# Optimization experiments

Hardware: AMD Instinct MI355X
Metric: run time of the kernel (lower is better)

## Reference

```python
import jax, jax.numpy as jnp
import numpy as np

NEG_SLOPE = 0.2  # PyG GATConv default leaky_relu slope


def gat_layer(x, src, dst, W, a_src, a_dst, bias, heads, d, concat):
    # x: [N, in_dim]; src/dst: [E] (edges flow src -> dst, self-loops included)
    N = x.shape[0]
    h = (x @ W).reshape(N, heads, d)                      # [N, H, D]
    alpha_src = jnp.einsum('nhd,hd->nh', h, a_src)        # [N, H]
    alpha_dst = jnp.einsum('nhd,hd->nh', h, a_dst)        # [N, H]
    e = jax.nn.leaky_relu(alpha_src[src] + alpha_dst[dst], NEG_SLOPE)  # [E, H]
    # softmax over incoming edges of each destination node (segment softmax)
    m = jax.ops.segment_max(e, dst, num_segments=N)       # [N, H]
    ex = jnp.exp(e - m[dst])
    s = jax.ops.segment_sum(ex, dst, num_segments=N)      # [N, H]
    alpha = ex / s[dst]                                   # [E, H]
    msg = h[src] * alpha[..., None]                       # [E, H, D]
    out = jax.ops.segment_sum(msg, dst, num_segments=N)   # [N, H, D]
    out = out.reshape(N, heads * d) if concat else out.mean(axis=1)
    return out + bias


def setup_inputs() -> dict:
    key = jax.random.key(0)
    ks = jax.random.split(key, 12)
    N, E = 10000, 320000
    in_dim, hidden, heads, out_dim = 256, 64, 4, 40
    x = jax.random.normal(ks[0], (N, in_dim), dtype=jnp.float32)
    edge_index = jax.random.randint(ks[1], (2, E), 0, N, dtype=jnp.int64)
    s = 0.1
    return {
        'x': x,
        'edge_index': edge_index,
        'W1': jax.random.normal(ks[2], (in_dim, heads * hidden), jnp.float32) * s,
        'att_src1': jax.random.normal(ks[3], (heads, hidden), jnp.float32) * s,
        'att_dst1': jax.random.normal(ks[4], (heads, hidden), jnp.float32) * s,
        'bias1': jnp.zeros((heads * hidden,), jnp.float32),
        'W2': jax.random.normal(ks[5], (heads * hidden, out_dim), jnp.float32) * s,
        'att_src2': jax.random.normal(ks[6], (1, out_dim), jnp.float32) * s,
        'att_dst2': jax.random.normal(ks[7], (1, out_dim), jnp.float32) * s,
        'bias2': jnp.zeros((out_dim,), jnp.float32),
    }


def reference(x, edge_index, W1, att_src1, att_dst1, bias1, W2, att_src2, att_dst2, bias2):
    N = x.shape[0]
    # PyG GATConv adds self-loops by default
    loop = jnp.arange(N, dtype=edge_index.dtype)
    src = jnp.concatenate([edge_index[0], loop])
    dst = jnp.concatenate([edge_index[1], loop])
    h = gat_layer(x, src, dst, W1, att_src1, att_dst1, bias1, heads=4, d=64, concat=True)
    h = jax.nn.relu(h)
    out = gat_layer(h, src, dst, W2, att_src2, att_dst2, bias2, heads=1, d=40, concat=False)
    return jax.nn.log_softmax(out, axis=1)
```

## Files before the change

kernel.cpp:

```cpp
#include <hip/hip_runtime.h>
#include <hip/hip_bf16.h>
#include <math.h>

#define IN_DIM 256
#define C1 256
#define H1 4
#define OUT_DIM 40
#define W2PAD 48
#define NEG_SLOPE 0.2f
#define DSTRIDE 128

typedef __attribute__((ext_vector_type(8))) short bf16x8;
typedef __attribute__((ext_vector_type(4))) float f32x4;
typedef __attribute__((ext_vector_type(2))) float f32x2;

#define XS_LD 264

__device__ __forceinline__ unsigned short f2bf(float f) {
    union { float f; unsigned u; } c; c.f = f;
    unsigned r = c.u + 0x7fffu + ((c.u >> 16) & 1u);
    return (unsigned short)(r >> 16);
}

__device__ __forceinline__ unsigned char f2fp8(float f) {
    return (unsigned char)__builtin_amdgcn_cvt_pk_fp8_f32(f, 0.f, 0, false);
}

__device__ __forceinline__ float sel4(float4 v, int h) {
    float r = v.x;
    r = (h == 1) ? v.y : r;
    r = (h == 2) ? v.z : r;
    r = (h == 3) ? v.w : r;
    return r;
}

__device__ __forceinline__ float leaky(float v) {
    return (v >= 0.0f) ? v : NEG_SLOPE * v;
}

__global__ void k_prep(int* __restrict__ fill, const float* __restrict__ W1,
                       unsigned short* __restrict__ W1t, const float* __restrict__ W2,
                       unsigned short* __restrict__ W2t, const float* __restrict__ a_src2,
                       const float* __restrict__ a_dst2, float* __restrict__ w2s,
                       float* __restrict__ w2d, int N) {
    int t = threadIdx.x;
    int g = blockIdx.x * 256 + t;
    if (g < N) fill[g] = 0;
    if (g < C1) {
        float s = 0.0f, d = 0.0f;
#pragma unroll
        for (int j = 0; j < OUT_DIM; ++j) {
            float w = W2[g * OUT_DIM + j];
            s += w * a_src2[j];
            d += w * a_dst2[j];
        }
        w2s[g] = s;
        w2d[g] = d;
    }
    if (g < W2PAD * C1) {
        int j = g >> 8, k = g & 255;
        W2t[g] = (j < OUT_DIM) ? f2bf(W2[k * OUT_DIM + j]) : 0;
    }
    __shared__ float s32[32][33];
    int b = blockIdx.x;
    int r0 = (b >> 3) * 32;
    int c0 = (b & 7) * 32;
    for (int i = t; i < 1024; i += 256) {
        int lr = i >> 5, lc = i & 31;
        s32[lr][lc] = W1[(r0 + lr) * 256 + c0 + lc];
    }
    __syncthreads();
    for (int i = t; i < 1024; i += 256) {
        int oc = i >> 5, ok = i & 31;
        W1t[(c0 + oc) * 256 + r0 + ok] = f2bf(s32[ok][oc]);
    }
}

__global__ void __launch_bounds__(256) k_fused1(
    const float* __restrict__ x, const unsigned short* __restrict__ W1t,
    const float* __restrict__ a_src, const float* __restrict__ a_dst,
    unsigned char* __restrict__ h1, float* __restrict__ as1, float* __restrict__ ad1,
    const int* __restrict__ ei, int* __restrict__ fill, unsigned short* __restrict__ srcs,
    int N, int E, int ET, int G1) {
    __shared__ unsigned short xs[64 * XS_LD];
    int t = threadIdx.x;

    if (blockIdx.x >= G1) {
        int e = (blockIdx.x - G1) * 256 + t;
        if (e < ET) {
            int s, d;
            if (e < E) { s = ei[e]; d = ei[E + e]; }
            else       { s = e - E; d = s; }
            int pos = atomicAdd(&fill[d], 1);
            srcs[(d << 7) + pos] = (unsigned short)s;
        }
        return;
    }

    int n0 = blockIdx.x * 64;
    for (int i = t; i < 4096; i += 256) {
        int r = i >> 6, c4 = i & 63;
        int n = n0 + r;
        float4 v = (n < N) ? ((const float4*)x)[(size_t)n * 64 + c4]
                           : make_float4(0.f, 0.f, 0.f, 0.f);
        uint2 pk;
        pk.x = (unsigned)f2bf(v.x) | ((unsigned)f2bf(v.y) << 16);
        pk.y = (unsigned)f2bf(v.z) | ((unsigned)f2bf(v.w) << 16);
        *((uint2*)&xs[r * XS_LD + c4 * 4]) = pk;
    }
    __syncthreads();

    int wv = t >> 6, lane = t & 63;
    int quad = lane >> 4, ln = lane & 15;

    f32x4 acc[4][4];
#pragma unroll
    for (int mt = 0; mt < 4; ++mt)
#pragma unroll
        for (int nt = 0; nt < 4; ++nt) acc[mt][nt] = (f32x4){0.f, 0.f, 0.f, 0.f};

#pragma unroll
    for (int kb = 0; kb < 8; ++kb) {
        bf16x8 af[4], bf[4];
#pragma unroll
        for (int mt = 0; mt < 4; ++mt)
            af[mt] = *((bf16x8*)&xs[(mt * 16 + ln) * XS_LD + kb * 32 + quad * 8]);
#pragma unroll
        for (int nt = 0; nt < 4; ++nt)
            bf[nt] = *((const bf16x8*)(W1t + ((wv * 64 + nt * 16 + ln) * 256 + kb * 32 + quad * 8)));
#pragma unroll
        for (int mt = 0; mt < 4; ++mt)
#pragma unroll
            for (int nt = 0; nt < 4; ++nt)
                acc[mt][nt] = __builtin_amdgcn_mfma_f32_16x16x32_bf16(af[mt], bf[nt], acc[mt][nt], 0, 0, 0);
    }

    float asv[4], adv[4];
#pragma unroll
    for (int nt = 0; nt < 4; ++nt) {
        int col = wv * 64 + nt * 16 + ln;
        asv[nt] = a_src[col];
        adv[nt] = a_dst[col];
    }
#pragma unroll
    for (int mt = 0; mt < 4; ++mt) {
        float ds[4] = {0.f, 0.f, 0.f, 0.f};
        float dd[4] = {0.f, 0.f, 0.f, 0.f};
#pragma unroll
        for (int nt = 0; nt < 4; ++nt) {
            int col = wv * 64 + nt * 16 + ln;
#pragma unroll
            for (int r = 0; r < 4; ++r) {
                int node = n0 + mt * 16 + quad * 4 + r;
                float v = acc[mt][nt][r];
                if (node < N) h1[(size_t)node * C1 + col] = f2fp8(v);
                ds[r] += v * asv[nt];
                dd[r] += v * adv[nt];
            }
        }
#pragma unroll
        for (int r = 0; r < 4; ++r) {
            float vs = ds[r], vd = dd[r];
#pragma unroll
            for (int o = 1; o < 16; o <<= 1) {
                vs += __shfl_xor(vs, o);
                vd += __shfl_xor(vd, o);
            }
            if (ln == 0) {
                int node = n0 + mt * 16 + quad * 4 + r;
                if (node < N) {
                    as1[node * H1 + wv] = vs;
                    ad1[node * H1 + wv] = vd;
                }
            }
        }
    }
}

__global__ void __launch_bounds__(256) k_node1(
    const int* __restrict__ fill, const unsigned short* __restrict__ srcs,
    const float* __restrict__ as1f, const float* __restrict__ ad1f,
    const unsigned char* __restrict__ h1, const float* __restrict__ bias1,
    const float* __restrict__ w2s, const float* __restrict__ w2d,
    unsigned short* __restrict__ agg1b, float* __restrict__ as2,
    float* __restrict__ ad2, int N) {
    int w = threadIdx.x >> 6, lane = threadIdx.x & 63;
    int n = blockIdx.x * 4 + w;
    if (n >= N) return;
    __shared__ float4 es[4][64];
    int start = n << 7;
    int end = start + fill[n];
    const float4* as4 = (const float4*)as1f;
    float4 adn = ((const float4*)ad1f)[n];
    int h = lane >> 4;
    const float* esw = (const float*)&es[w][0];

    float4 S4 = make_float4(0.f, 0.f, 0.f, 0.f);
    float ac0 = 0.f, ac1 = 0.f, ac2 = 0.f, ac3 = 0.f;

    for (int c = start; c < end; c += 64) {
        int cnt = min(64, end - c);
        int idx = c + lane;
        int sreg = (idx < end) ? (int)srcs[idx] : 0;
        float4 ex = make_float4(0.f, 0.f, 0.f, 0.f);
        if (idx < end) {
            float4 a = as4[sreg];
            ex.x = __expf(leaky(a.x + adn.x));
            ex.y = __expf(leaky(a.y + adn.y));
            ex.z = __expf(leaky(a.z + adn.z));
            ex.w = __expf(leaky(a.w + adn.w));
        }
        S4.x += ex.x; S4.y += ex.y; S4.z += ex.z; S4.w += ex.w;
        es[w][lane] = ex;

        int i = 0;
        for (; i + 7 < cnt; i += 8) {
            int s[8]; float a[8]; unsigned r[8];
#pragma unroll
            for (int k = 0; k < 8; ++k) {
                s[k] = __shfl(sreg, i + k);
                a[k] = esw[(i + k) * 4 + h];
            }
#pragma unroll
            for (int k = 0; k < 8; ++k)
                r[k] = ((const unsigned*)(h1 + (size_t)s[k] * C1))[lane];
#pragma unroll
            for (int k = 0; k < 8; ++k) {
                f32x2 lo = __builtin_amdgcn_cvt_pk_f32_fp8(r[k], false);
                f32x2 hi = __builtin_amdgcn_cvt_pk_f32_fp8(r[k], true);
                ac0 += a[k] * lo.x;
                ac1 += a[k] * lo.y;
                ac2 += a[k] * hi.x;
                ac3 += a[k] * hi.y;
            }
        }
        for (; i < cnt; ++i) {
            int s0 = __shfl(sreg, i);
            float a0 = esw[i * 4 + h];
            unsigned r0 = ((const unsigned*)(h1 + (size_t)s0 * C1))[lane];
            f32x2 lo = __builtin_amdgcn_cvt_pk_f32_fp8(r0, false);
            f32x2 hi = __builtin_amdgcn_cvt_pk_f32_fp8(r0, true);
            ac0 += a0 * lo.x;
            ac1 += a0 * lo.y;
            ac2 += a0 * hi.x;
            ac3 += a0 * hi.y;
        }
    }

#pragma unroll
    for (int o = 32; o > 0; o >>= 1) {
        S4.x += __shfl_xor(S4.x, o);
        S4.y += __shfl_xor(S4.y, o);
        S4.z += __shfl_xor(S4.z, o);
        S4.w += __shfl_xor(S4.w, o);
    }
    float iS = 1.0f / sel4(S4, h);
    float4 b = ((const float4*)bias1)[lane];
    float v0 = fmaxf(ac0 * iS + b.x, 0.f);
    float v1 = fmaxf(ac1 * iS + b.y, 0.f);
    float v2 = fmaxf(ac2 * iS + b.z, 0.f);
    float v3 = fmaxf(ac3 * iS + b.w, 0.f);
    uint2 pk;
    pk.x = (unsigned)f2bf(v0) | ((unsigned)f2bf(v1) << 16);
    pk.y = (unsigned)f2bf(v2) | ((unsigned)f2bf(v3) << 16);
    ((uint2*)(agg1b + (size_t)n * C1))[lane] = pk;

    float4 ws = ((const float4*)w2s)[lane];
    float4 wd = ((const float4*)w2d)[lane];
    float ps = v0 * ws.x + v1 * ws.y + v2 * ws.z + v3 * ws.w;
    float pd = v0 * wd.x + v1 * wd.y + v2 * wd.z + v3 * wd.w;
#pragma unroll
    for (int o = 32; o > 0; o >>= 1) {
        ps += __shfl_xor(ps, o);
        pd += __shfl_xor(pd, o);
    }
    if (lane == 0) { as2[n] = ps; ad2[n] = pd; }
}

__global__ void __launch_bounds__(256) k_gemm2m(
    const unsigned short* __restrict__ agg1b, const unsigned short* __restrict__ W2t,
    unsigned short* __restrict__ h2b, int N) {
    int t = threadIdx.x;
    int wv = t >> 6, lane = t & 63;
    int quad = lane >> 4, ln = lane & 15;
    int n0 = blockIdx.x * 64;
    int mrow = n0 + wv * 16 + ln;

    f32x4 acc[3];
#pragma unroll
    for (int nt = 0; nt < 3; ++nt) acc[nt] = (f32x4){0.f, 0.f, 0.f, 0.f};

#pragma unroll
    for (int kb = 0; kb < 8; ++kb) {
        bf16x8 af = *((const bf16x8*)(agg1b + (size_t)mrow * C1 + kb * 32 + quad * 8));
#pragma unroll
        for (int nt = 0; nt < 3; ++nt) {
            bf16x8 bfr = *((const bf16x8*)(W2t + ((nt * 16 + ln) * C1 + kb * 32 + quad * 8)));
            acc[nt] = __builtin_amdgcn_mfma_f32_16x16x32_bf16(af, bfr, acc[nt], 0, 0, 0);
        }
    }
#pragma unroll
    for (int nt = 0; nt < 3; ++nt) {
        int col = nt * 16 + ln;
        if (col < OUT_DIM) {
#pragma unroll
            for (int r = 0; r < 4; ++r) {
                int node = n0 + wv * 16 + quad * 4 + r;
                if (node < N) h2b[(size_t)node * OUT_DIM + col] = f2bf(acc[nt][r]);
            }
        }
    }
}

__global__ void __launch_bounds__(256) k_node2(
    const int* __restrict__ fill, const unsigned short* __restrict__ srcs,
    const float* __restrict__ as2, const float* __restrict__ ad2,
    const unsigned short* __restrict__ h2b, const float* __restrict__ bias2,
    float* __restrict__ out, int N) {
    int w = threadIdx.x >> 6, lane = threadIdx.x & 63;
    int n = blockIdx.x * 4 + w;
    if (n >= N) return;
    int start = n << 7;
    int end = start + fill[n];
    float adn = ad2[n];
    float S = 0.f, acc0 = 0.f, acc1 = 0.f;
    bool act = lane < 20;

    for (int c = start; c < end; c += 64) {
        int cnt = min(64, end - c);
        int idx = c + lane;
        int sreg = (idx < end) ? (int)srcs[idx] : 0;
        float ex = (idx < end) ? __expf(leaky(as2[sreg] + adn)) : 0.f;
        S += ex;
        int i = 0;
        for (; i + 3 < cnt; i += 4) {
            int su[4]; float al[4]; unsigned rw[4];
#pragma unroll
            for (int k = 0; k < 4; ++k) {
                su[k] = __shfl(sreg, i + k);
                al[k] = __shfl(ex, i + k);
            }
#pragma unroll
            for (int k = 0; k < 4; ++k)
                rw[k] = act ? *(const unsigned*)(h2b + (size_t)su[k] * OUT_DIM + lane * 2) : 0u;
#pragma unroll
            for (int k = 0; k < 4; ++k) {
                acc0 += al[k] * __uint_as_float(rw[k] << 16);
                acc1 += al[k] * __uint_as_float(rw[k] & 0xffff0000u);
            }
        }
        for (; i < cnt; ++i) {
            int su0 = __shfl(sreg, i);
            float al0 = __shfl(ex, i);
            unsigned rw0 = act ? *(const unsigned*)(h2b + (size_t)su0 * OUT_DIM + lane * 2) : 0u;
            acc0 += al0 * __uint_as_float(rw0 << 16);
            acc1 += al0 * __uint_as_float(rw0 & 0xffff0000u);
        }
    }
#pragma unroll
    for (int o = 32; o > 0; o >>= 1) S += __shfl_xor(S, o);

    float v0 = act ? (acc0 / S + bias2[lane * 2]) : -INFINITY;
    float v1 = act ? (acc1 / S + bias2[lane * 2 + 1]) : -INFINITY;
    float mx = fmaxf(v0, v1);
#pragma unroll
    for (int o = 16; o > 0; o >>= 1) mx = fmaxf(mx, __shfl_xor(mx, o));
    float e0 = act ? __expf(v0 - mx) : 0.f;
    float e1 = act ? __expf(v1 - mx) : 0.f;
    float esum = e0 + e1;
#pragma unroll
    for (int o = 16; o > 0; o >>= 1) esum += __shfl_xor(esum, o);
    if (act) {
        float l = mx + logf(esum);
        out[(size_t)n * OUT_DIM + lane * 2]     = v0 - l;
        out[(size_t)n * OUT_DIM + lane * 2 + 1] = v1 - l;
    }
}

extern "C" void kernel_launch(void* const* d_in, const int* in_sizes, int n_in,
                              void* d_out, int out_size, void* d_ws, size_t ws_size,
                              hipStream_t stream) {
    const float* x        = (const float*)d_in[0];
    const int*   ei       = (const int*)d_in[1];
    const float* W1       = (const float*)d_in[2];
    const float* att_src1 = (const float*)d_in[3];
    const float* att_dst1 = (const float*)d_in[4];
    const float* bias1    = (const float*)d_in[5];
    const float* W2       = (const float*)d_in[6];
    const float* att_src2 = (const float*)d_in[7];
    const float* att_dst2 = (const float*)d_in[8];
    const float* bias2    = (const float*)d_in[9];
    float* out = (float*)d_out;

    const int N  = in_sizes[0] / IN_DIM;
    const int E  = in_sizes[1] / 2;
    const int ET = E + N;
    const int Npad = (N + 63) & ~63;

    char* base = (char*)d_ws;
    auto alloc = [&](size_t bytes) {
        char* p = base;
        base += (bytes + 255) & ~(size_t)255;
        return p;
    };
    unsigned char*  h1    = (unsigned char*)alloc((size_t)N * C1);
    unsigned short* W1t   = (unsigned short*)alloc((size_t)C1 * C1 * 2);
    unsigned short* W2t   = (unsigned short*)alloc((size_t)W2PAD * C1 * 2);
    unsigned short* agg1b = (unsigned short*)alloc((size_t)Npad * C1 * 2);
    unsigned short* h2b   = (unsigned short*)alloc((size_t)N * OUT_DIM * 2);
    float* as1   = (float*)alloc((size_t)N * H1 * 4);
    float* ad1   = (float*)alloc((size_t)N * H1 * 4);
    float* as2   = (float*)alloc((size_t)N * 4);
    float* ad2   = (float*)alloc((size_t)N * 4);
    float* w2s   = (float*)alloc((size_t)C1 * 4);
    float* w2d   = (float*)alloc((size_t)C1 * 4);
    int* fill    = (int*)alloc((size_t)N * 4);
    unsigned short* srcs = (unsigned short*)alloc((size_t)N * DSTRIDE * 2);

    const int G1 = (N + 63) / 64;
    const int GS = (ET + 255) / 256;

    k_prep<<<64, 256, 0, stream>>>(fill, W1, W1t, W2, W2t, att_src2, att_dst2, w2s, w2d, N);
    k_fused1<<<G1 + GS, 256, 0, stream>>>(x, W1t, att_src1, att_dst1, h1, as1, ad1,
                                          ei, fill, srcs, N, E, ET, G1);
    k_node1<<<(N + 3) / 4, 256, 0, stream>>>(fill, srcs, as1, ad1, h1, bias1, w2s, w2d,
                                             agg1b, as2, ad2, N);
    k_gemm2m<<<(N + 63) / 64, 256, 0, stream>>>(agg1b, W2t, h2b, N);
    k_node2<<<(N + 3) / 4, 256, 0, stream>>>(fill, srcs, as2, ad2, h2b, bias2, out, N);
}
```

Baseline: 149.6 us.

## Pad fill counters, batch edge scatter per thread, stage h1 stores through LDS

Spreads the per-node atomic fill counters to one every 64 bytes to cut atomic contention and false sharing between neighbouring nodes. Each scatter thread now handles four edges, so fewer scatter blocks are launched. The fp8 h1 tile is written to shared memory first and then stored to global memory as coalesced 16-byte vectors instead of scattered byte stores. The cost is a 16x larger fill buffer, strided fill reads in the node kernels, and two extra barriers in the GEMM blocks.

```diff
diff --git a/kernel.cpp b/kernel.cpp
--- a/kernel.cpp
+++ b/kernel.cpp
@@ -45,7 +45,7 @@
                        float* __restrict__ w2d, int N) {
     int t = threadIdx.x;
     int g = blockIdx.x * 256 + t;
-    if (g < N) fill[g] = 0;
+    if (g < N) fill[g << 4] = 0;
     if (g < C1) {
         float s = 0.0f, d = 0.0f;
 #pragma unroll
@@ -86,13 +86,17 @@
     int t = threadIdx.x;
 
     if (blockIdx.x >= G1) {
-        int e = (blockIdx.x - G1) * 256 + t;
-        if (e < ET) {
-            int s, d;
-            if (e < E) { s = ei[e]; d = ei[E + e]; }
-            else       { s = e - E; d = s; }
-            int pos = atomicAdd(&fill[d], 1);
-            srcs[(d << 7) + pos] = (unsigned short)s;
+        int eb = (blockIdx.x - G1) * 1024 + t;
+#pragma unroll
+        for (int k = 0; k < 4; ++k) {
+            int e = eb + k * 256;
+            if (e < ET) {
+                int s, d;
+                if (e < E) { s = ei[e]; d = ei[E + e]; }
+                else       { s = e - E; d = s; }
+                int pos = atomicAdd(&fill[d << 4], 1);
+                srcs[(d << 7) + pos] = (unsigned short)s;
+            }
         }
         return;
     }
@@ -148,12 +152,9 @@
         float dd[4] = {0.f, 0.f, 0.f, 0.f};
 #pragma unroll
         for (int nt = 0; nt < 4; ++nt) {
-            int col = wv * 64 + nt * 16 + ln;
 #pragma unroll
             for (int r = 0; r < 4; ++r) {
-                int node = n0 + mt * 16 + quad * 4 + r;
                 float v = acc[mt][nt][r];
-                if (node < N) h1[(size_t)node * C1 + col] = f2fp8(v);
                 ds[r] += v * asv[nt];
                 dd[r] += v * adv[nt];
             }
@@ -174,6 +175,23 @@
                 }
             }
         }
+    }
+
+    __syncthreads();
+    unsigned char* bt = (unsigned char*)xs;
+#pragma unroll
+    for (int mt = 0; mt < 4; ++mt)
+#pragma unroll
+        for (int nt = 0; nt < 4; ++nt)
+#pragma unroll
+            for (int r = 0; r < 4; ++r)
+                bt[(mt * 16 + quad * 4 + r) * 256 + wv * 64 + nt * 16 + ln] = f2fp8(acc[mt][nt][r]);
+    __syncthreads();
+    const uint4* bt4 = (const uint4*)bt;
+    uint4* h14 = (uint4*)(h1 + (size_t)n0 * C1);
+    for (int i = t; i < 1024; i += 256) {
+        int row = i >> 4;
+        if (n0 + row < N) h14[i] = bt4[i];
     }
 }
 
@@ -189,7 +207,7 @@
     if (n >= N) return;
     __shared__ float4 es[4][64];
     int start = n << 7;
-    int end = start + fill[n];
+    int end = start + fill[n << 4];
     const float4* as4 = (const float4*)as1f;
     float4 adn = ((const float4*)ad1f)[n];
     int h = lane >> 4;
@@ -321,7 +339,7 @@
     int n = blockIdx.x * 4 + w;
     if (n >= N) return;
     int start = n << 7;
-    int end = start + fill[n];
+    int end = start + fill[n << 4];
     float adn = ad2[n];
     float S = 0.f, acc0 = 0.f, acc1 = 0.f;
     bool act = lane < 20;
@@ -414,11 +432,11 @@
     float* ad2   = (float*)alloc((size_t)N * 4);
     float* w2s   = (float*)alloc((size_t)C1 * 4);
     float* w2d   = (float*)alloc((size_t)C1 * 4);
-    int* fill    = (int*)alloc((size_t)N * 4);
+    int* fill    = (int*)alloc((size_t)N * 16 * 4);
     unsigned short* srcs = (unsigned short*)alloc((size_t)N * DSTRIDE * 2);
 
     const int G1 = (N + 63) / 64;
-    const int GS = (ET + 255) / 256;
+    const int GS = (ET + 1023) / 1024;
 
     k_prep<<<64, 256, 0, stream>>>(fill, W1, W1t, W2, W2t, att_src2, att_dst2, w2s, w2d, N);
     k_fused1<<<G1 + GS, 256, 0, stream>>>(x, W1t, att_src1, att_dst1, h1, as1, ad1,
```

New measurement: 142.6 us. -4.7%, faster.
